# Optimization experiments

Hardware: AMD Instinct MI355X
Metric: run time of the kernel (lower is better)

## Reference

```python
import jax, jax.numpy as jnp
import numpy as np

B, S, D, H, O, E, K = 4, 2048, 1024, 2048, 1024, 8, 2

def setup_inputs() -> dict:
    key = jax.random.key(0)
    ks = jax.random.split(key, 8)
    x = jax.random.normal(ks[0], (B, S, D), dtype=jnp.float32)
    # kaiming-uniform-ish scale for weights, zero biases (as in _init_w)
    gate_w = jax.random.uniform(ks[1], (E, D), dtype=jnp.float32, minval=-1, maxval=1) * np.sqrt(6.0 / D)
    gate_b = jnp.zeros((E,), dtype=jnp.float32)
    w1 = jax.random.uniform(ks[2], (E, D, H), dtype=jnp.float32, minval=-1, maxval=1) * np.sqrt(6.0 / D)
    b1 = jnp.zeros((E, H), dtype=jnp.float32)
    w2 = jax.random.uniform(ks[3], (E, H, O), dtype=jnp.float32, minval=-1, maxval=1) * np.sqrt(6.0 / H)
    b2 = jnp.zeros((E, O), dtype=jnp.float32)
    return {"x": x, "gate_w": gate_w, "gate_b": gate_b, "w1": w1, "b1": b1, "w2": w2, "b2": b2}

def reference(x, gate_w, gate_b, w1, b1, w2, b2):
    # gate: softmax over experts, then top-k (k=2)
    logits = jnp.einsum('bsd,ed->bse', x, gate_w) + gate_b          # [B,S,E]
    probs = jax.nn.softmax(logits, axis=-1)
    topk_vals, topk_idx = jax.lax.top_k(probs, K)                    # [B,S,K]
    # dense all-expert MLPs (Linear-ReLU-Linear), dropout = 0
    h = jax.nn.relu(jnp.einsum('bsd,edh->bseh', x, w1) + b1)         # [B,S,E,H]
    expert_out = jnp.einsum('bseh,eho->bseo', h, w2) + b2            # [B,S,E,O]
    # gather top-k experts and combine with gate weights
    sel = jnp.take_along_axis(expert_out, topk_idx[..., None], axis=2)  # [B,S,K,O]
    return jnp.sum(sel * topk_vals[..., None], axis=2)               # [B,S,O]
```

## Files before the change

kernel.cpp:

```cpp
#include <hip/hip_runtime.h>

#define T_TOKENS 8192
#define D_DIM 1024
#define H_DIM 2048
#define O_DIM 1024
#define E_NUM 8
#define NPAIR 16384

typedef unsigned short u16;
typedef __bf16 bf16x8 __attribute__((ext_vector_type(8)));
typedef float f32x4 __attribute__((ext_vector_type(4)));

__device__ inline u16 f2bf(float f) {
  union { float f; unsigned u; } v; v.f = f;
  unsigned r = v.u + 0x7FFFu + ((v.u >> 16) & 1u);
  return (u16)(r >> 16);
}

__device__ __forceinline__ void gload16(const u16* g, u16* l) {
  __builtin_amdgcn_global_load_lds((const __attribute__((address_space(1))) void*)g,
                                   (__attribute__((address_space(3))) void*)l, 16, 0, 0);
}

__global__ void cvt_x_kernel(const float* __restrict__ x, u16* __restrict__ xb) {
  int i = (blockIdx.x * 256 + threadIdx.x) * 4;
  float4 v = *(const float4*)(x + i);
  ushort4 o;
  o.x = f2bf(v.x); o.y = f2bf(v.y); o.z = f2bf(v.z); o.w = f2bf(v.w);
  *(ushort4*)(xb + i) = o;
}

__global__ void transpose_cvt_kernel(const float* __restrict__ w, u16* __restrict__ wt,
                                     int R, int C) {
  __shared__ float tile[32][33];
  int e = blockIdx.z;
  int c0 = blockIdx.x * 32, r0 = blockIdx.y * 32;
  const float* wp = w + (size_t)e * R * C;
  u16* wtp = wt + (size_t)e * R * C;
  int tx = threadIdx.x, ty = threadIdx.y;
  #pragma unroll
  for (int j = 0; j < 32; j += 8)
    tile[ty + j][tx] = wp[(size_t)(r0 + ty + j) * C + c0 + tx];
  __syncthreads();
  #pragma unroll
  for (int j = 0; j < 32; j += 8)
    wtp[(size_t)(c0 + ty + j) * R + r0 + tx] = f2bf(tile[tx][ty + j]);
}

__global__ void gate_kernel(const float* __restrict__ x, const float* __restrict__ gw,
                            const float* __restrict__ gb, int* __restrict__ topk_idx,
                            float* __restrict__ topk_val) {
  int t = blockIdx.x * 4 + (threadIdx.x >> 6);
  int lane = threadIdx.x & 63;
  const float4* xr4 = (const float4*)(x + (size_t)t * D_DIM);
  const float4* gw4 = (const float4*)gw;
  float acc[E_NUM];
  #pragma unroll
  for (int e = 0; e < E_NUM; e++) acc[e] = 0.f;
  #pragma unroll
  for (int it = 0; it < D_DIM / 256; ++it) {
    float4 xv = xr4[it * 64 + lane];
    #pragma unroll
    for (int e = 0; e < E_NUM; e++) {
      float4 wv = gw4[e * (D_DIM / 4) + it * 64 + lane];
      acc[e] += xv.x * wv.x + xv.y * wv.y + xv.z * wv.z + xv.w * wv.w;
    }
  }
  #pragma unroll
  for (int e = 0; e < E_NUM; e++) {
    #pragma unroll
    for (int o = 32; o > 0; o >>= 1) acc[e] += __shfl_down(acc[e], o);
  }
  if (lane == 0) {
    float l[E_NUM], mx = -1e30f;
    #pragma unroll
    for (int e = 0; e < E_NUM; e++) { l[e] = acc[e] + gb[e]; mx = fmaxf(mx, l[e]); }
    float p[E_NUM], s = 0.f;
    #pragma unroll
    for (int e = 0; e < E_NUM; e++) { p[e] = expf(l[e] - mx); s += p[e]; }
    float inv = 1.f / s;
    int i1 = 0;
    #pragma unroll
    for (int e = 1; e < E_NUM; e++) if (p[e] > p[i1]) i1 = e;
    int i2 = (i1 == 0) ? 1 : 0;
    #pragma unroll
    for (int e = 0; e < E_NUM; e++) if (e != i1 && e != i2 && p[e] > p[i2]) i2 = e;
    topk_idx[t * 2] = i1;     topk_idx[t * 2 + 1] = i2;
    topk_val[t * 2] = p[i1] * inv; topk_val[t * 2 + 1] = p[i2] * inv;
  }
}

__global__ void histscan_kernel(const int* __restrict__ topk_idx,
                                int* __restrict__ counts, int* __restrict__ eoff) {
  __shared__ int wh[4][E_NUM];
  int tid = threadIdx.x;
  int lane = tid & 63, wave = tid >> 6;
  int myc = 0;
  for (int i = tid; i < NPAIR; i += 256) {
    int e = topk_idx[i];
    #pragma unroll
    for (int ee = 0; ee < E_NUM; ee++) {
      unsigned long long m = __ballot(e == ee);
      if (lane == ee) myc += __popcll(m);
    }
  }
  if (lane < E_NUM) wh[wave][lane] = myc;
  __syncthreads();
  if (tid == 0) {
    int s = 0;
    for (int e = 0; e < E_NUM; e++) {
      int c = wh[0][e] + wh[1][e] + wh[2][e] + wh[3][e];
      counts[e] = c;
      eoff[e] = s;
      s += c;
    }
    eoff[E_NUM] = s;
  }
}

__global__ void scatter_kernel(const int* __restrict__ topk_idx, const float* __restrict__ topk_val,
                               const int* __restrict__ eoff, int* __restrict__ cursor_pad,
                               int* __restrict__ pair_token, float* __restrict__ pair_gate) {
  __shared__ int lhist[E_NUM];
  __shared__ int lbase[E_NUM];
  int tid = threadIdx.x;
  int t = blockIdx.x * 256 + tid;
  if (tid < E_NUM) lhist[tid] = 0;
  __syncthreads();
  int e0 = topk_idx[t * 2], e1 = topk_idx[t * 2 + 1];
  int r0 = atomicAdd(&lhist[e0], 1);
  int r1 = atomicAdd(&lhist[e1], 1);
  __syncthreads();
  if (tid < E_NUM) lbase[tid] = eoff[tid] + atomicAdd(&cursor_pad[tid * 32], lhist[tid]);
  __syncthreads();
  int p0 = lbase[e0] + r0;
  int p1 = lbase[e1] + r1;
  pair_token[p0] = t; pair_gate[p0] = topk_val[t * 2];
  pair_token[p1] = t; pair_gate[p1] = topk_val[t * 2 + 1];
}


__global__ __launch_bounds__(256, 3) void gemm1_kernel(
    const u16* __restrict__ xb, const u16* __restrict__ w1t, const float* __restrict__ b1,
    const int* __restrict__ pair_token, const int* __restrict__ eoff,
    const int* __restrict__ ecnt, u16* __restrict__ hbuf) {
  const int e = blockIdx.z;
  const int ne = ecnt[e];
  const int m0t = blockIdx.y * 128;
  if (m0t >= ne) return;
  const int off = eoff[e];
  const int n0 = blockIdx.x * 128;

  __shared__ __align__(16) u16 As[128 * 32];
  __shared__ __align__(16) u16 Bs[128 * 32];

  const int tid = threadIdx.x;
  const int wid = tid >> 6;
  const int lane = tid & 63;

  const int strow = lane >> 2;
  const int gsw = (lane & 3) ^ ((lane >> 3) & 3);
  const int r0 = wid * 32 + strow;
  const int r1 = r0 + 16;
  int gm0 = m0t + r0, gm1 = m0t + r1;
  int tok0 = (gm0 < ne) ? pair_token[off + gm0] : 0;
  int tok1 = (gm1 < ne) ? pair_token[off + gm1] : 0;
  const u16* a0 = xb + (size_t)tok0 * D_DIM + gsw * 8;
  const u16* a1 = xb + (size_t)tok1 * D_DIM + gsw * 8;
  const u16* bp0 = w1t + ((size_t)e * H_DIM + (n0 + r0)) * D_DIM + gsw * 8;
  const u16* bp1 = w1t + ((size_t)e * H_DIM + (n0 + r1)) * D_DIM + gsw * 8;
  u16* lA0 = As + wid * 1024;
  u16* lA1 = As + wid * 1024 + 512;
  u16* lB0 = Bs + wid * 1024;
  u16* lB1 = Bs + wid * 1024 + 512;

  const int wm = (wid & 1) * 64;
  const int wn = (wid >> 1) * 64;
  const int lrow = lane & 15;
  const int quad = lane >> 4;
  const int gq = quad ^ ((lrow >> 1) & 3);

  f32x4 acc[4][4] = {};

  for (int k0 = 0; k0 < D_DIM; k0 += 32) {
    gload16(a0 + k0, lA0);
    gload16(a1 + k0, lA1);
    gload16(bp0 + k0, lB0);
    gload16(bp1 + k0, lB1);
    __syncthreads();
    bf16x8 af[4], bfr[4];
    #pragma unroll
    for (int i = 0; i < 4; i++) af[i] = *(const bf16x8*)&As[(wm + i * 16 + lrow) * 32 + gq * 8];
    #pragma unroll
    for (int j = 0; j < 4; j++) bfr[j] = *(const bf16x8*)&Bs[(wn + j * 16 + lrow) * 32 + gq * 8];
    #pragma unroll
    for (int i = 0; i < 4; i++)
      #pragma unroll
      for (int j = 0; j < 4; j++)
        acc[i][j] = __builtin_amdgcn_mfma_f32_16x16x32_bf16(af[i], bfr[j], acc[i][j], 0, 0, 0);
    __syncthreads();
  }
  #pragma unroll
  for (int i = 0; i < 4; i++) {
    #pragma unroll
    for (int r = 0; r < 4; r++) {
      int m = wm + i * 16 + quad * 4 + r;
      int gm = m0t + m;
      if (gm >= ne) continue;
      size_t rowbase = (size_t)(off + gm) * H_DIM;
      #pragma unroll
      for (int j = 0; j < 4; j++) {
        int n = n0 + wn + j * 16 + lrow;
        float v = acc[i][j][r] + b1[e * H_DIM + n];
        v = v > 0.f ? v : 0.f;
        hbuf[rowbase + n] = f2bf(v);
      }
    }
  }
}

__global__ __launch_bounds__(256, 3) void gemm2_kernel(
    const u16* __restrict__ hbuf, const u16* __restrict__ w2t, const float* __restrict__ b2,
    const int* __restrict__ pair_token, const float* __restrict__ pair_gate,
    const int* __restrict__ eoff, const int* __restrict__ ecnt, float* __restrict__ out) {
  const int e = blockIdx.z;
  const int ne = ecnt[e];
  const int m0t = blockIdx.y * 128;
  if (m0t >= ne) return;
  const int off = eoff[e];
  const int n0 = blockIdx.x * 128;

  __shared__ __align__(16) u16 As[128 * 32];
  __shared__ __align__(16) u16 Bs[128 * 32];

  const int tid = threadIdx.x;
  const int wid = tid >> 6;
  const int lane = tid & 63;

  const int strow = lane >> 2;
  const int gsw = (lane & 3) ^ ((lane >> 3) & 3);
  const int r0 = wid * 32 + strow;
  const int r1 = r0 + 16;
  const u16* a0 = hbuf + (size_t)(off + m0t + r0) * H_DIM + gsw * 8;
  const u16* a1 = hbuf + (size_t)(off + m0t + r1) * H_DIM + gsw * 8;
  const u16* bp0 = w2t + ((size_t)e * O_DIM + (n0 + r0)) * H_DIM + gsw * 8;
  const u16* bp1 = w2t + ((size_t)e * O_DIM + (n0 + r1)) * H_DIM + gsw * 8;
  u16* lA0 = As + wid * 1024;
  u16* lA1 = As + wid * 1024 + 512;
  u16* lB0 = Bs + wid * 1024;
  u16* lB1 = Bs + wid * 1024 + 512;

  const int wm = (wid & 1) * 64;
  const int wn = (wid >> 1) * 64;
  const int lrow = lane & 15;
  const int quad = lane >> 4;
  const int gq = quad ^ ((lrow >> 1) & 3);

  f32x4 acc[4][4] = {};

  for (int k0 = 0; k0 < H_DIM; k0 += 32) {
    gload16(a0 + k0, lA0);
    gload16(a1 + k0, lA1);
    gload16(bp0 + k0, lB0);
    gload16(bp1 + k0, lB1);
    __syncthreads();
    bf16x8 af[4], bfr[4];
    #pragma unroll
    for (int i = 0; i < 4; i++) af[i] = *(const bf16x8*)&As[(wm + i * 16 + lrow) * 32 + gq * 8];
    #pragma unroll
    for (int j = 0; j < 4; j++) bfr[j] = *(const bf16x8*)&Bs[(wn + j * 16 + lrow) * 32 + gq * 8];
    #pragma unroll
    for (int i = 0; i < 4; i++)
      #pragma unroll
      for (int j = 0; j < 4; j++)
        acc[i][j] = __builtin_amdgcn_mfma_f32_16x16x32_bf16(af[i], bfr[j], acc[i][j], 0, 0, 0);
    __syncthreads();
  }
  #pragma unroll
  for (int i = 0; i < 4; i++) {
    #pragma unroll
    for (int r = 0; r < 4; r++) {
      int m = wm + i * 16 + quad * 4 + r;
      int gm = m0t + m;
      if (gm >= ne) continue;
      int pair = off + gm;
      int tok = pair_token[pair];
      float g = pair_gate[pair];
      #pragma unroll
      for (int j = 0; j < 4; j++) {
        int n = n0 + wn + j * 16 + lrow;
        float v = (acc[i][j][r] + b2[e * O_DIM + n]) * g;
        atomicAdd(&out[(size_t)tok * O_DIM + n], v);
      }
    }
  }
}

extern "C" void kernel_launch(void* const* d_in, const int* in_sizes, int n_in,
                              void* d_out, int out_size, void* d_ws, size_t ws_size,
                              hipStream_t stream) {
  const float* x  = (const float*)d_in[0];
  const float* gw = (const float*)d_in[1];
  const float* gb = (const float*)d_in[2];
  const float* w1 = (const float*)d_in[3];
  const float* b1 = (const float*)d_in[4];
  const float* w2 = (const float*)d_in[5];
  const float* b2 = (const float*)d_in[6];
  float* out = (float*)d_out;

  char* ws = (char*)d_ws;
  size_t off = 0;
  auto take = [&](size_t bytes) -> char* {
    char* p = ws + off;
    off = (off + bytes + 255) & ~(size_t)255;
    return p;
  };
  int*   meta       = (int*)take(2048);
  int*   cursor_pad = meta;
  int*   counts     = meta + 256;
  int*   eoff       = meta + 264;
  int*   topk_idx   = (int*)take((size_t)T_TOKENS * 2 * 4);
  float* topk_val   = (float*)take((size_t)T_TOKENS * 2 * 4);
  int*   pair_token = (int*)take((size_t)(NPAIR + 256) * 4);
  float* pair_gate  = (float*)take((size_t)(NPAIR + 256) * 4);
  u16*   xb         = (u16*)take((size_t)T_TOKENS * D_DIM * 2);
  u16*   w1t        = (u16*)take((size_t)E_NUM * D_DIM * H_DIM * 2);
  u16*   w2t        = (u16*)take((size_t)E_NUM * H_DIM * O_DIM * 2);
  u16*   hbuf       = (u16*)take((size_t)(NPAIR + 128) * H_DIM * 2);

  hipMemsetAsync(meta, 0, 2048, stream);
  hipMemsetAsync(out, 0, (size_t)T_TOKENS * O_DIM * 4, stream);

  cvt_x_kernel<<<(T_TOKENS * D_DIM) / (256 * 4), 256, 0, stream>>>(x, xb);
  transpose_cvt_kernel<<<dim3(H_DIM / 32, D_DIM / 32, E_NUM), dim3(32, 8), 0, stream>>>(w1, w1t, D_DIM, H_DIM);
  transpose_cvt_kernel<<<dim3(O_DIM / 32, H_DIM / 32, E_NUM), dim3(32, 8), 0, stream>>>(w2, w2t, H_DIM, O_DIM);
  gate_kernel<<<T_TOKENS / 4, 256, 0, stream>>>(x, gw, gb, topk_idx, topk_val);
  histscan_kernel<<<1, 256, 0, stream>>>(topk_idx, counts, eoff);
  scatter_kernel<<<T_TOKENS / 256, 256, 0, stream>>>(topk_idx, topk_val, eoff, cursor_pad, pair_token, pair_gate);
  gemm1_kernel<<<dim3(H_DIM / 128, NPAIR / 128, E_NUM), 256, 0, stream>>>(xb, w1t, b1, pair_token, eoff, counts, hbuf);
  gemm2_kernel<<<dim3(O_DIM / 128, NPAIR / 128, E_NUM), 256, 0, stream>>>(hbuf, w2t, b2, pair_token, pair_gate, eoff, counts, out);
}
```

Before: 528.5 us.

## Double-buffer GEMM LDS tiles, fuse x conversion into gate, reorder grid

Both expert GEMMs now use double-buffered LDS tiles. The next K-slice is prefetched with global_load_lds while MFMAs run on the current one, which drops one barrier per iteration. The bf16 conversion of x moves into the gate kernel, removing a separate launch and a second read of x. The grid is reordered so the M tile is on blockIdx.x, and the occupancy hint rises to 4. LDS per block doubles, and the single barrier per iteration depends on the hardware's load-to-LDS ordering guarantees for correctness.

```diff
diff --git a/kernel.cpp b/kernel.cpp
--- a/kernel.cpp
+++ b/kernel.cpp
@@ -20,14 +20,6 @@
 __device__ __forceinline__ void gload16(const u16* g, u16* l) {
   __builtin_amdgcn_global_load_lds((const __attribute__((address_space(1))) void*)g,
                                    (__attribute__((address_space(3))) void*)l, 16, 0, 0);
-}
-
-__global__ void cvt_x_kernel(const float* __restrict__ x, u16* __restrict__ xb) {
-  int i = (blockIdx.x * 256 + threadIdx.x) * 4;
-  float4 v = *(const float4*)(x + i);
-  ushort4 o;
-  o.x = f2bf(v.x); o.y = f2bf(v.y); o.z = f2bf(v.z); o.w = f2bf(v.w);
-  *(ushort4*)(xb + i) = o;
 }
 
 __global__ void transpose_cvt_kernel(const float* __restrict__ w, u16* __restrict__ wt,
@@ -49,17 +41,21 @@
 
 __global__ void gate_kernel(const float* __restrict__ x, const float* __restrict__ gw,
                             const float* __restrict__ gb, int* __restrict__ topk_idx,
-                            float* __restrict__ topk_val) {
+                            float* __restrict__ topk_val, u16* __restrict__ xb) {
   int t = blockIdx.x * 4 + (threadIdx.x >> 6);
   int lane = threadIdx.x & 63;
   const float4* xr4 = (const float4*)(x + (size_t)t * D_DIM);
   const float4* gw4 = (const float4*)gw;
+  u16* xbr = xb + (size_t)t * D_DIM;
   float acc[E_NUM];
   #pragma unroll
   for (int e = 0; e < E_NUM; e++) acc[e] = 0.f;
   #pragma unroll
   for (int it = 0; it < D_DIM / 256; ++it) {
     float4 xv = xr4[it * 64 + lane];
+    ushort4 o;
+    o.x = f2bf(xv.x); o.y = f2bf(xv.y); o.z = f2bf(xv.z); o.w = f2bf(xv.w);
+    *(ushort4*)(xbr + (it * 64 + lane) * 4) = o;
     #pragma unroll
     for (int e = 0; e < E_NUM; e++) {
       float4 wv = gw4[e * (D_DIM / 4) + it * 64 + lane];
@@ -140,19 +136,19 @@
 }
 
 
-__global__ __launch_bounds__(256, 3) void gemm1_kernel(
+__global__ __launch_bounds__(256, 4) void gemm1_kernel(
     const u16* __restrict__ xb, const u16* __restrict__ w1t, const float* __restrict__ b1,
     const int* __restrict__ pair_token, const int* __restrict__ eoff,
     const int* __restrict__ ecnt, u16* __restrict__ hbuf) {
   const int e = blockIdx.z;
   const int ne = ecnt[e];
-  const int m0t = blockIdx.y * 128;
+  const int m0t = blockIdx.x * 128;
   if (m0t >= ne) return;
   const int off = eoff[e];
-  const int n0 = blockIdx.x * 128;
-
-  __shared__ __align__(16) u16 As[128 * 32];
-  __shared__ __align__(16) u16 Bs[128 * 32];
+  const int n0 = blockIdx.y * 128;
+
+  __shared__ __align__(16) u16 As[2 * 128 * 32];
+  __shared__ __align__(16) u16 Bs[2 * 128 * 32];
 
   const int tid = threadIdx.x;
   const int wid = tid >> 6;
@@ -169,10 +165,7 @@
   const u16* a1 = xb + (size_t)tok1 * D_DIM + gsw * 8;
   const u16* bp0 = w1t + ((size_t)e * H_DIM + (n0 + r0)) * D_DIM + gsw * 8;
   const u16* bp1 = w1t + ((size_t)e * H_DIM + (n0 + r1)) * D_DIM + gsw * 8;
-  u16* lA0 = As + wid * 1024;
-  u16* lA1 = As + wid * 1024 + 512;
-  u16* lB0 = Bs + wid * 1024;
-  u16* lB1 = Bs + wid * 1024 + 512;
+  const int dep = wid * 1024;
 
   const int wm = (wid & 1) * 64;
   const int wn = (wid >> 1) * 64;
@@ -182,23 +175,30 @@
 
   f32x4 acc[4][4] = {};
 
+  gload16(a0, As + dep);       gload16(a1, As + dep + 512);
+  gload16(bp0, Bs + dep);      gload16(bp1, Bs + dep + 512);
+
+  int p = 0;
   for (int k0 = 0; k0 < D_DIM; k0 += 32) {
-    gload16(a0 + k0, lA0);
-    gload16(a1 + k0, lA1);
-    gload16(bp0 + k0, lB0);
-    gload16(bp1 + k0, lB1);
     __syncthreads();
+    int kn = k0 + 32;
+    if (kn < D_DIM) {
+      int qb = (p ^ 1) * 4096;
+      gload16(a0 + kn, As + qb + dep);   gload16(a1 + kn, As + qb + dep + 512);
+      gload16(bp0 + kn, Bs + qb + dep);  gload16(bp1 + kn, Bs + qb + dep + 512);
+    }
+    const int base = p * 4096;
     bf16x8 af[4], bfr[4];
     #pragma unroll
-    for (int i = 0; i < 4; i++) af[i] = *(const bf16x8*)&As[(wm + i * 16 + lrow) * 32 + gq * 8];
-    #pragma unroll
-    for (int j = 0; j < 4; j++) bfr[j] = *(const bf16x8*)&Bs[(wn + j * 16 + lrow) * 32 + gq * 8];
+    for (int i = 0; i < 4; i++) af[i] = *(const bf16x8*)&As[base + (wm + i * 16 + lrow) * 32 + gq * 8];
+    #pragma unroll
+    for (int j = 0; j < 4; j++) bfr[j] = *(const bf16x8*)&Bs[base + (wn + j * 16 + lrow) * 32 + gq * 8];
     #pragma unroll
     for (int i = 0; i < 4; i++)
       #pragma unroll
       for (int j = 0; j < 4; j++)
         acc[i][j] = __builtin_amdgcn_mfma_f32_16x16x32_bf16(af[i], bfr[j], acc[i][j], 0, 0, 0);
-    __syncthreads();
+    p ^= 1;
   }
   #pragma unroll
   for (int i = 0; i < 4; i++) {
@@ -219,19 +219,19 @@
   }
 }
 
-__global__ __launch_bounds__(256, 3) void gemm2_kernel(
+__global__ __launch_bounds__(256, 4) void gemm2_kernel(
     const u16* __restrict__ hbuf, const u16* __restrict__ w2t, const float* __restrict__ b2,
     const int* __restrict__ pair_token, const float* __restrict__ pair_gate,
     const int* __restrict__ eoff, const int* __restrict__ ecnt, float* __restrict__ out) {
   const int e = blockIdx.z;
   const int ne = ecnt[e];
-  const int m0t = blockIdx.y * 128;
+  const int m0t = blockIdx.x * 128;
   if (m0t >= ne) return;
   const int off = eoff[e];
-  const int n0 = blockIdx.x * 128;
-
-  __shared__ __align__(16) u16 As[128 * 32];
-  __shared__ __align__(16) u16 Bs[128 * 32];
+  const int n0 = blockIdx.y * 128;
+
+  __shared__ __align__(16) u16 As[2 * 128 * 32];
+  __shared__ __align__(16) u16 Bs[2 * 128 * 32];
 
   const int tid = threadIdx.x;
   const int wid = tid >> 6;
@@ -245,10 +245,7 @@
   const u16* a1 = hbuf + (size_t)(off + m0t + r1) * H_DIM + gsw * 8;
   const u16* bp0 = w2t + ((size_t)e * O_DIM + (n0 + r0)) * H_DIM + gsw * 8;
   const u16* bp1 = w2t + ((size_t)e * O_DIM + (n0 + r1)) * H_DIM + gsw * 8;
-  u16* lA0 = As + wid * 1024;
-  u16* lA1 = As + wid * 1024 + 512;
-  u16* lB0 = Bs + wid * 1024;
-  u16* lB1 = Bs + wid * 1024 + 512;
+  const int dep = wid * 1024;
 
   const int wm = (wid & 1) * 64;
   const int wn = (wid >> 1) * 64;
@@ -258,23 +255,30 @@
 
   f32x4 acc[4][4] = {};
 
+  gload16(a0, As + dep);       gload16(a1, As + dep + 512);
+  gload16(bp0, Bs + dep);      gload16(bp1, Bs + dep + 512);
+
+  int p = 0;
   for (int k0 = 0; k0 < H_DIM; k0 += 32) {
-    gload16(a0 + k0, lA0);
-    gload16(a1 + k0, lA1);
-    gload16(bp0 + k0, lB0);
-    gload16(bp1 + k0, lB1);
     __syncthreads();
+    int kn = k0 + 32;
+    if (kn < H_DIM) {
+      int qb = (p ^ 1) * 4096;
+      gload16(a0 + kn, As + qb + dep);   gload16(a1 + kn, As + qb + dep + 512);
+      gload16(bp0 + kn, Bs + qb + dep);  gload16(bp1 + kn, Bs + qb + dep + 512);
+    }
+    const int base = p * 4096;
     bf16x8 af[4], bfr[4];
     #pragma unroll
-    for (int i = 0; i < 4; i++) af[i] = *(const bf16x8*)&As[(wm + i * 16 + lrow) * 32 + gq * 8];
-    #pragma unroll
-    for (int j = 0; j < 4; j++) bfr[j] = *(const bf16x8*)&Bs[(wn + j * 16 + lrow) * 32 + gq * 8];
+    for (int i = 0; i < 4; i++) af[i] = *(const bf16x8*)&As[base + (wm + i * 16 + lrow) * 32 + gq * 8];
+    #pragma unroll
+    for (int j = 0; j < 4; j++) bfr[j] = *(const bf16x8*)&Bs[base + (wn + j * 16 + lrow) * 32 + gq * 8];
     #pragma unroll
     for (int i = 0; i < 4; i++)
       #pragma unroll
       for (int j = 0; j < 4; j++)
         acc[i][j] = __builtin_amdgcn_mfma_f32_16x16x32_bf16(af[i], bfr[j], acc[i][j], 0, 0, 0);
-    __syncthreads();
+    p ^= 1;
   }
   #pragma unroll
   for (int i = 0; i < 4; i++) {
@@ -331,12 +335,11 @@
   hipMemsetAsync(meta, 0, 2048, stream);
   hipMemsetAsync(out, 0, (size_t)T_TOKENS * O_DIM * 4, stream);
 
-  cvt_x_kernel<<<(T_TOKENS * D_DIM) / (256 * 4), 256, 0, stream>>>(x, xb);
   transpose_cvt_kernel<<<dim3(H_DIM / 32, D_DIM / 32, E_NUM), dim3(32, 8), 0, stream>>>(w1, w1t, D_DIM, H_DIM);
   transpose_cvt_kernel<<<dim3(O_DIM / 32, H_DIM / 32, E_NUM), dim3(32, 8), 0, stream>>>(w2, w2t, H_DIM, O_DIM);
-  gate_kernel<<<T_TOKENS / 4, 256, 0, stream>>>(x, gw, gb, topk_idx, topk_val);
+  gate_kernel<<<T_TOKENS / 4, 256, 0, stream>>>(x, gw, gb, topk_idx, topk_val, xb);
   histscan_kernel<<<1, 256, 0, stream>>>(topk_idx, counts, eoff);
   scatter_kernel<<<T_TOKENS / 256, 256, 0, stream>>>(topk_idx, topk_val, eoff, cursor_pad, pair_token, pair_gate);
-  gemm1_kernel<<<dim3(H_DIM / 128, NPAIR / 128, E_NUM), 256, 0, stream>>>(xb, w1t, b1, pair_token, eoff, counts, hbuf);
-  gemm2_kernel<<<dim3(O_DIM / 128, NPAIR / 128, E_NUM), 256, 0, stream>>>(hbuf, w2t, b2, pair_token, pair_gate, eoff, counts, out);
-}
+  gemm1_kernel<<<dim3(NPAIR / 128, H_DIM / 128, E_NUM), 256, 0, stream>>>(xb, w1t, b1, pair_token, eoff, counts, hbuf);
+  gemm2_kernel<<<dim3(NPAIR / 128, O_DIM / 128, E_NUM), 256, 0, stream>>>(hbuf, w2t, b2, pair_token, pair_gate, eoff, counts, out);
+}
```

New measurement: 639.7 us. 21.0% more time.
